# Performance work log

Hardware: AMD Instinct MI355X
Metric: run time of the kernel (lower is better)

Reference implementation:

```python
import jax, jax.numpy as jnp
import numpy as np

N = 50000      # nodes
E = 1600000    # edges (avg degree 32)
F_IN = 3       # PROTEINS num_node_features
H = 64         # dim_h
G = 512        # num graphs in batch
C = 2          # PROTEINS num_classes
BN_EPS = 1e-5


def setup_inputs() -> dict:
    key = jax.random.key(0)
    ks = iter(jax.random.split(key, 64))

    def rn(shape, s=0.1):
        return (jax.random.normal(next(ks), shape) * s).astype(jnp.float32)

    inp = {"x": rn((N, F_IN), 1.0)}
    for li, din in ((1, F_IN), (2, H), (3, H)):
        p = f"conv{li}_"
        inp[p + "w1"] = rn((din, H))
        inp[p + "b1"] = rn((H,))
        inp[p + "bn_g"] = jnp.ones((H,), jnp.float32)
        inp[p + "bn_b"] = jnp.zeros((H,), jnp.float32)
        inp[p + "bn_m"] = rn((H,))
        inp[p + "bn_v"] = jax.random.uniform(next(ks), (H,), jnp.float32, 0.5, 1.5)
        inp[p + "w2"] = rn((H, H))
        inp[p + "b2"] = rn((H,))
    inp["lin1_w"] = rn((3 * H, 3 * H))
    inp["lin1_b"] = rn((3 * H,))
    inp["lin2_w"] = rn((3 * H, C))
    inp["lin2_b"] = rn((C,))
    inp["edge_index"] = jax.random.randint(next(ks), (2, E), 0, N, jnp.int64)
    inp["batch"] = jnp.sort(jax.random.randint(next(ks), (N,), 0, G, jnp.int64))
    return inp


def gin_conv(x, src, dst, w1, b1, g, bb, m, v, w2, b2):
    # GINConv, eps=0: mlp(x + sum_{j->i} x_j); aggregate messages at target (dst)
    agg = jax.ops.segment_sum(x[src], dst, num_segments=N)  # [N, d]
    h = x + agg
    h = h @ w1 + b1
    h = (h - m) * jax.lax.rsqrt(v + BN_EPS) * g + bb  # BatchNorm1d (eval)
    h = jax.nn.relu(h)
    h = jax.nn.relu(h @ w2 + b2)
    return h


def reference(x,
              conv1_w1, conv1_b1, conv1_bn_g, conv1_bn_b, conv1_bn_m, conv1_bn_v, conv1_w2, conv1_b2,
              conv2_w1, conv2_b1, conv2_bn_g, conv2_bn_b, conv2_bn_m, conv2_bn_v, conv2_w2, conv2_b2,
              conv3_w1, conv3_b1, conv3_bn_g, conv3_bn_b, conv3_bn_m, conv3_bn_v, conv3_w2, conv3_b2,
              lin1_w, lin1_b, lin2_w, lin2_b,
              edge_index, batch):
    src, dst = edge_index[0], edge_index[1]
    h1 = gin_conv(x,  src, dst, conv1_w1, conv1_b1, conv1_bn_g, conv1_bn_b, conv1_bn_m, conv1_bn_v, conv1_w2, conv1_b2)
    h2 = gin_conv(h1, src, dst, conv2_w1, conv2_b1, conv2_bn_g, conv2_bn_b, conv2_bn_m, conv2_bn_v, conv2_w2, conv2_b2)
    h3 = gin_conv(h2, src, dst, conv3_w1, conv3_b1, conv3_bn_g, conv3_bn_b, conv3_bn_m, conv3_bn_v, conv3_w2, conv3_b2)
    # global_add_pool per graph
    p1 = jax.ops.segment_sum(h1, batch, num_segments=G)
    p2 = jax.ops.segment_sum(h2, batch, num_segments=G)
    p3 = jax.ops.segment_sum(h3, batch, num_segments=G)
    h = jnp.concatenate((p1, p2, p3), axis=1)          # [G, 3H]
    h = jax.nn.relu(h @ lin1_w + lin1_b)
    # dropout p=0.5 is identity in eval mode
    h = h @ lin2_w + lin2_b                            # [G, C]
    return (h, jax.nn.log_softmax(h, axis=1))
```

## Files before the change

### kernel.cpp

```cpp
#include <hip/hip_runtime.h>
#include <hip/hip_bf16.h>
#include <math.h>

#define N_NODES 50000
#define N_EDGES 1600000
#define H 64
#define G_GRAPHS 512
#define C_CLS 2
#define BN_EPS 1e-5f
#define NBUCK 196
#define E4 (N_EDGES / 4)
#define CSR_BLOCKS ((E4 + 511) / 512)

typedef __attribute__((ext_vector_type(8))) short short8;
typedef __attribute__((ext_vector_type(4))) float floatx4;

__device__ __forceinline__ float bflo(unsigned int u) { return __uint_as_float(u << 16); }
__device__ __forceinline__ float bfhi(unsigned int u) { return __uint_as_float(u & 0xffff0000u); }
__device__ __forceinline__ unsigned int bf16_rne(float f) {
    unsigned int u = __float_as_uint(f);
    u += 0x7fffu + ((u >> 16) & 1u);
    return u >> 16;
}

__global__ __launch_bounds__(256) void bhist_kernel(const int* __restrict__ dst,
                                                    int* __restrict__ gbh) {
    __shared__ int bh[NBUCK];
    int t = threadIdx.x;
    if (t < NBUCK) bh[t] = 0;
    __syncthreads();
    int base = blockIdx.x * 512;
#pragma unroll
    for (int p = 0; p < 2; p++) {
        int i = base + p * 256 + t;
        if (i < E4) {
            int4 d = ((const int4*)dst)[i];
            atomicAdd(&bh[d.x >> 8], 1);
            atomicAdd(&bh[d.y >> 8], 1);
            atomicAdd(&bh[d.z >> 8], 1);
            atomicAdd(&bh[d.w >> 8], 1);
        }
    }
    __syncthreads();
    if (t < NBUCK && bh[t]) atomicAdd(&gbh[t], bh[t]);
}

__global__ __launch_bounds__(256) void bscan_kernel(const int* __restrict__ gbh,
                                                    int* __restrict__ bucket_start,
                                                    int* __restrict__ cursor,
                                                    int* __restrict__ row_start) {
    __shared__ int s[256];
    int t = threadIdx.x;
    int v = (t < NBUCK) ? gbh[t] : 0;
    s[t] = v;
    __syncthreads();
    for (int off = 1; off < 256; off <<= 1) {
        int u = 0;
        if (t >= off) u = s[t - off];
        __syncthreads();
        if (t >= off) s[t] += u;
        __syncthreads();
    }
    int excl = s[t] - v;
    if (t < NBUCK) { bucket_start[t] = excl; cursor[t] = excl; }
    if (t == 0) { bucket_start[NBUCK] = N_EDGES; row_start[N_NODES] = N_EDGES; }
}

__global__ __launch_bounds__(256) void bscatter_kernel(const int* __restrict__ src,
                                                       const int* __restrict__ dst,
                                                       int* __restrict__ cursor,
                                                       int* __restrict__ gpacked) {
    __shared__ int bh[NBUCK];
    int t = threadIdx.x;
    if (t < NBUCK) bh[t] = 0;
    __syncthreads();
    int base = blockIdx.x * 512;

    int pkA[4], bkA[4], lrA[4]; bool vA = false;
    int pkB[4], bkB[4], lrB[4]; bool vB = false;
    {
        int i = base + t;
        if (i < E4) {
            vA = true;
            int4 s4 = ((const int4*)src)[i];
            int4 d4 = ((const int4*)dst)[i];
            bkA[0] = d4.x >> 8; pkA[0] = ((d4.x & 255) << 16) | s4.x; lrA[0] = atomicAdd(&bh[bkA[0]], 1);
            bkA[1] = d4.y >> 8; pkA[1] = ((d4.y & 255) << 16) | s4.y; lrA[1] = atomicAdd(&bh[bkA[1]], 1);
            bkA[2] = d4.z >> 8; pkA[2] = ((d4.z & 255) << 16) | s4.z; lrA[2] = atomicAdd(&bh[bkA[2]], 1);
            bkA[3] = d4.w >> 8; pkA[3] = ((d4.w & 255) << 16) | s4.w; lrA[3] = atomicAdd(&bh[bkA[3]], 1);
        }
    }
    {
        int i = base + 256 + t;
        if (i < E4) {
            vB = true;
            int4 s4 = ((const int4*)src)[i];
            int4 d4 = ((const int4*)dst)[i];
            bkB[0] = d4.x >> 8; pkB[0] = ((d4.x & 255) << 16) | s4.x; lrB[0] = atomicAdd(&bh[bkB[0]], 1);
            bkB[1] = d4.y >> 8; pkB[1] = ((d4.y & 255) << 16) | s4.y; lrB[1] = atomicAdd(&bh[bkB[1]], 1);
            bkB[2] = d4.z >> 8; pkB[2] = ((d4.z & 255) << 16) | s4.z; lrB[2] = atomicAdd(&bh[bkB[2]], 1);
            bkB[3] = d4.w >> 8; pkB[3] = ((d4.w & 255) << 16) | s4.w; lrB[3] = atomicAdd(&bh[bkB[3]], 1);
        }
    }
    __syncthreads();
    if (t < NBUCK) {
        int c = bh[t];
        bh[t] = c ? atomicAdd(&cursor[t], c) : 0;
    }
    __syncthreads();
    if (vA) {
#pragma unroll
        for (int q = 0; q < 4; q++) gpacked[bh[bkA[q]] + lrA[q]] = pkA[q];
    }
    if (vB) {
#pragma unroll
        for (int q = 0; q < 4; q++) gpacked[bh[bkB[q]] + lrB[q]] = pkB[q];
    }
}

__global__ __launch_bounds__(256) void bcsr_kernel(const int* __restrict__ gpacked,
                                                   const int* __restrict__ bucket_start,
                                                   int* __restrict__ row_start,
                                                   int* __restrict__ edge_src) {
    __shared__ int cnt[256];
    __shared__ int pref[256];
    int b = blockIdx.x;
    int t = threadIdx.x;
    int bs = bucket_start[b], be = bucket_start[b + 1];
    cnt[t] = 0;
    __syncthreads();
    for (int i = bs + t; i < be; i += 256) atomicAdd(&cnt[gpacked[i] >> 16], 1);
    __syncthreads();
    int v = cnt[t];
    pref[t] = v;
    __syncthreads();
    for (int off = 1; off < 256; off <<= 1) {
        int u = 0;
        if (t >= off) u = pref[t - off];
        __syncthreads();
        if (t >= off) pref[t] += u;
        __syncthreads();
    }
    int excl = pref[t] - v;
    int node = b * 256 + t;
    if (node < N_NODES) row_start[node] = bs + excl;
    cnt[t] = excl;
    __syncthreads();
    for (int i = bs + t; i < be; i += 256) {
        int p = gpacked[i];
        int pos = atomicAdd(&cnt[p >> 16], 1);
        edge_src[bs + pos] = p & 0xffff;
    }
}

__global__ __launch_bounds__(256) void gin_layer3_kernel(
    const float* __restrict__ x, const int* __restrict__ row_start,
    const int* __restrict__ edge_src,
    const float* __restrict__ w1, const float* __restrict__ b1,
    const float* __restrict__ bn_g, const float* __restrict__ bn_b,
    const float* __restrict__ bn_m, const float* __restrict__ bn_v,
    const float* __restrict__ w2, const float* __restrict__ b2,
    __hip_bfloat16* __restrict__ hout) {
    __shared__ float s_w1[3 * H];
    __shared__ float s_w2[H * H];
    __shared__ float s_mid[4][H];
    __shared__ float s_scale[H], s_shift[H], s_b1[H], s_b2[H];

    int tid = threadIdx.x;
    for (int i = tid; i < 3 * H; i += 256) s_w1[i] = w1[i];
    for (int i = tid; i < H * H; i += 256) s_w2[i] = w2[i];
    if (tid < H) {
        float sc = rsqrtf(bn_v[tid] + BN_EPS) * bn_g[tid];
        s_scale[tid] = sc;
        s_shift[tid] = bn_b[tid] - bn_m[tid] * sc;
        s_b1[tid] = b1[tid];
        s_b2[tid] = b2[tid];
    }
    __syncthreads();

    int wave = tid >> 6;
    int j = tid & 63;
    int node = blockIdx.x * 4 + wave;

    int rs = row_start[node], re = row_start[node + 1];
    float a0 = 0.f, a1 = 0.f, a2 = 0.f;
    for (int t = rs + j; t < re; t += 64) {
        int s = edge_src[t];
        a0 += x[s * 3 + 0];
        a1 += x[s * 3 + 1];
        a2 += x[s * 3 + 2];
    }
#pragma unroll
    for (int off = 32; off > 0; off >>= 1) {
        a0 += __shfl_xor(a0, off);
        a1 += __shfl_xor(a1, off);
        a2 += __shfl_xor(a2, off);
    }
    float in0 = a0 + x[node * 3 + 0];
    float in1 = a1 + x[node * 3 + 1];
    float in2 = a2 + x[node * 3 + 2];

    float m = s_b1[j] + in0 * s_w1[0 * H + j] + in1 * s_w1[1 * H + j] + in2 * s_w1[2 * H + j];
    m = m * s_scale[j] + s_shift[j];
    m = fmaxf(m, 0.f);
    s_mid[wave][j] = m;
    __syncthreads();
    float o = s_b2[j];
#pragma unroll
    for (int k = 0; k < H; k++) o += s_mid[wave][k] * s_w2[k * H + j];
    o = fmaxf(o, 0.f);
    hout[(size_t)node * H + j] = __float2bfloat16(o);
}

__global__ __launch_bounds__(512) void gather_kernel(
    const __hip_bfloat16* __restrict__ hin, const int* __restrict__ row_start,
    const int* __restrict__ edge_src, __hip_bfloat16* __restrict__ xs) {
    int tid = threadIdx.x;
    int wave = tid >> 6;
    int j = tid & 63;
    int o = j >> 3;
    int jo = j & 7;
    int node = blockIdx.x * 8 + wave;

    const char* hb = (const char*)hin;
    int rs = row_start[node], re = row_start[node + 1];
    float a0 = 0.f, a1 = 0.f, a2 = 0.f, a3 = 0.f, a4 = 0.f, a5 = 0.f, a6 = 0.f, a7 = 0.f;
    for (int base = rs; base < re; base += 64) {
        int idx = base + j;
        int sv = (idx < re) ? edge_src[idx] : 0;
        int cnt = min(64, re - base);
        int i = 0;
        for (; i + 8 <= cnt; i += 8) {
            int s = __shfl(sv, i + o);
            uint4 raw = *(const uint4*)(hb + (size_t)s * 128 + jo * 16);
            a0 += bflo(raw.x); a1 += bfhi(raw.x);
            a2 += bflo(raw.y); a3 += bfhi(raw.y);
            a4 += bflo(raw.z); a5 += bfhi(raw.z);
            a6 += bflo(raw.w); a7 += bfhi(raw.w);
        }
        if (i < cnt) {
            int r = cnt - i;
            int s = __shfl(sv, i + (o < r ? o : 0));
            uint4 raw = *(const uint4*)(hb + (size_t)s * 128 + jo * 16);
            if (o < r) {
                a0 += bflo(raw.x); a1 += bfhi(raw.x);
                a2 += bflo(raw.y); a3 += bfhi(raw.y);
                a4 += bflo(raw.z); a5 += bfhi(raw.z);
                a6 += bflo(raw.w); a7 += bfhi(raw.w);
            }
        }
    }
    a0 += __shfl_xor(a0, 8); a0 += __shfl_xor(a0, 16); a0 += __shfl_xor(a0, 32);
    a1 += __shfl_xor(a1, 8); a1 += __shfl_xor(a1, 16); a1 += __shfl_xor(a1, 32);
    a2 += __shfl_xor(a2, 8); a2 += __shfl_xor(a2, 16); a2 += __shfl_xor(a2, 32);
    a3 += __shfl_xor(a3, 8); a3 += __shfl_xor(a3, 16); a3 += __shfl_xor(a3, 32);
    a4 += __shfl_xor(a4, 8); a4 += __shfl_xor(a4, 16); a4 += __shfl_xor(a4, 32);
    a5 += __shfl_xor(a5, 8); a5 += __shfl_xor(a5, 16); a5 += __shfl_xor(a5, 32);
    a6 += __shfl_xor(a6, 8); a6 += __shfl_xor(a6, 16); a6 += __shfl_xor(a6, 32);
    a7 += __shfl_xor(a7, 8); a7 += __shfl_xor(a7, 16); a7 += __shfl_xor(a7, 32);
    if (o == 0) {
        uint4 raw = *(const uint4*)(hb + (size_t)node * 128 + jo * 16);
        a0 += bflo(raw.x); a1 += bfhi(raw.x);
        a2 += bflo(raw.y); a3 += bfhi(raw.y);
        a4 += bflo(raw.z); a5 += bfhi(raw.z);
        a6 += bflo(raw.w); a7 += bfhi(raw.w);
        uint4 ov;
        ov.x = bf16_rne(a0) | (bf16_rne(a1) << 16);
        ov.y = bf16_rne(a2) | (bf16_rne(a3) << 16);
        ov.z = bf16_rne(a4) | (bf16_rne(a5) << 16);
        ov.w = bf16_rne(a6) | (bf16_rne(a7) << 16);
        *(uint4*)((char*)xs + (size_t)node * 128 + jo * 16) = ov;
    }
}

#define IOP 72
__global__ __launch_bounds__(256) void mlp_mfma_kernel(
    const __hip_bfloat16* __restrict__ xs,
    const float* __restrict__ w1, const float* __restrict__ b1,
    const float* __restrict__ bn_g, const float* __restrict__ bn_b,
    const float* __restrict__ bn_m, const float* __restrict__ bn_v,
    const float* __restrict__ w2, const float* __restrict__ b2,
    __hip_bfloat16* __restrict__ hout) {
    __shared__ unsigned short s_w1t[H * IOP];
    __shared__ unsigned short s_w2t[H * IOP];
    __shared__ unsigned short s_mid[4][16 * IOP];
    __shared__ unsigned short s_out[4][16 * IOP];

    int tid = threadIdx.x;
    for (int idx = tid; idx < H * H; idx += 256) {
        int k = idx >> 6, jj = idx & 63;
        s_w1t[jj * IOP + k] = (unsigned short)bf16_rne(w1[idx]);
        s_w2t[jj * IOP + k] = (unsigned short)bf16_rne(w2[idx]);
    }
    int lane = tid & 63, wave = tid >> 6;
    int quad = lane >> 4, l15 = lane & 15;
    float scl[4], sht[4], bb1[4], bb2[4];
#pragma unroll
    for (int jt = 0; jt < 4; jt++) {
        int j = jt * 16 + l15;
        float sc = rsqrtf(bn_v[j] + BN_EPS) * bn_g[j];
        scl[jt] = sc;
        sht[jt] = bn_b[j] - bn_m[j] * sc;
        bb1[jt] = b1[j];
        bb2[jt] = b2[j];
    }
    __syncthreads();

    int base = blockIdx.x * 64 + wave * 16;
    const unsigned short* xr = (const unsigned short*)xs;
    int am = min(base + l15, N_NODES - 1);
    short8 a0 = *(const short8*)(xr + (size_t)am * H + quad * 8);
    short8 a1 = *(const short8*)(xr + (size_t)am * H + quad * 8 + 32);

    unsigned short* mid = s_mid[wave];
    unsigned short* outw = s_out[wave];

#pragma unroll
    for (int jt = 0; jt < 4; jt++) {
        short8 b0 = *(const short8*)&s_w1t[(jt * 16 + l15) * IOP + quad * 8];
        short8 bv = *(const short8*)&s_w1t[(jt * 16 + l15) * IOP + quad * 8 + 32];
        floatx4 c = {0.f, 0.f, 0.f, 0.f};
        c = __builtin_amdgcn_mfma_f32_16x16x32_bf16(a0, b0, c, 0, 0, 0);
        c = __builtin_amdgcn_mfma_f32_16x16x32_bf16(a1, bv, c, 0, 0, 0);
#pragma unroll
        for (int r = 0; r < 4; r++) {
            float v = (c[r] + bb1[jt]) * scl[jt] + sht[jt];
            v = fmaxf(v, 0.f);
            mid[(quad * 4 + r) * IOP + jt * 16 + l15] = (unsigned short)bf16_rne(v);
        }
    }
    __syncthreads();

    short8 m0 = *(const short8*)&mid[l15 * IOP + quad * 8];
    short8 m1 = *(const short8*)&mid[l15 * IOP + quad * 8 + 32];
#pragma unroll
    for (int jt = 0; jt < 4; jt++) {
        short8 b0 = *(const short8*)&s_w2t[(jt * 16 + l15) * IOP + quad * 8];
        short8 bv = *(const short8*)&s_w2t[(jt * 16 + l15) * IOP + quad * 8 + 32];
        floatx4 c = {0.f, 0.f, 0.f, 0.f};
        c = __builtin_amdgcn_mfma_f32_16x16x32_bf16(m0, b0, c, 0, 0, 0);
        c = __builtin_amdgcn_mfma_f32_16x16x32_bf16(m1, bv, c, 0, 0, 0);
#pragma unroll
        for (int r = 0; r < 4; r++) {
            float v = fmaxf(c[r] + bb2[jt], 0.f);
            outw[(quad * 4 + r) * IOP + jt * 16 + l15] = (unsigned short)bf16_rne(v);
        }
    }
    __syncthreads();

    unsigned short* ho = (unsigned short*)hout;
#pragma unroll
    for (int cc = 0; cc < 2; cc++) {
        int r = cc * 8 + (lane >> 3);
        int node = base + r;
        if (node < N_NODES) {
            short8 v = *(const short8*)&outw[r * IOP + (lane & 7) * 8];
            *(short8*)(ho + (size_t)node * H + (lane & 7) * 8) = v;
        }
    }
}

__global__ __launch_bounds__(192) void pool_head_kernel(
    const __hip_bfloat16* __restrict__ h1, const __hip_bfloat16* __restrict__ h2,
    const __hip_bfloat16* __restrict__ h3, const int* __restrict__ batch,
    const float* __restrict__ lin1_w, const float* __restrict__ lin1_b,
    const float* __restrict__ lin2_w, const float* __restrict__ lin2_b,
    float* __restrict__ out) {
    __shared__ float s_row[3 * H];
    __shared__ float s_mid[3 * H];
    __shared__ float s_z[C_CLS];
    __shared__ int s_se[2];

    int g = blockIdx.x;
    int j = threadIdx.x;
    if (j < 2) {
        int target = g + j;
        int lo = 0, hi = N_NODES;
        while (lo < hi) {
            int mid = (lo + hi) >> 1;
            if (batch[mid] < target) lo = mid + 1; else hi = mid;
        }
        s_se[j] = lo;
    }
    __syncthreads();
    int ns = s_se[0], ne = s_se[1];

    int which = j >> 6;
    int f = j & 63;
    const __hip_bfloat16* h = (which == 0) ? h1 : ((which == 1) ? h2 : h3);
    float p0 = 0.f, p1 = 0.f, p2 = 0.f, p3 = 0.f;
    int n = ns;
    for (; n + 3 < ne; n += 4) {
        p0 += __bfloat162float(h[(size_t)n * H + f]);
        p1 += __bfloat162float(h[(size_t)(n + 1) * H + f]);
        p2 += __bfloat162float(h[(size_t)(n + 2) * H + f]);
        p3 += __bfloat162float(h[(size_t)(n + 3) * H + f]);
    }
    for (; n < ne; n++) p0 += __bfloat162float(h[(size_t)n * H + f]);
    s_row[j] = (p0 + p1) + (p2 + p3);
    __syncthreads();

    float acc = lin1_b[j];
    for (int k = 0; k < 3 * H; k++) acc += s_row[k] * lin1_w[k * (3 * H) + j];
    s_mid[j] = fmaxf(acc, 0.f);
    __syncthreads();

    if (j < C_CLS) {
        float z = lin2_b[j];
        for (int k = 0; k < 3 * H; k++) z += s_mid[k] * lin2_w[k * C_CLS + j];
        s_z[j] = z;
    }
    __syncthreads();
    if (j < C_CLS) {
        float z0 = s_z[0], z1 = s_z[1];
        float mx = fmaxf(z0, z1);
        float lse = mx + logf(expf(z0 - mx) + expf(z1 - mx));
        out[g * C_CLS + j] = s_z[j];
        out[G_GRAPHS * C_CLS + g * C_CLS + j] = s_z[j] - lse;
    }
}

extern "C" void kernel_launch(void* const* d_in, const int* in_sizes, int n_in,
                              void* d_out, int out_size, void* d_ws, size_t ws_size,
                              hipStream_t stream) {
    const float* x = (const float*)d_in[0];
    const float* cw1[3], *cb1[3], *cg[3], *cbb[3], *cm[3], *cv[3], *cw2[3], *cb2[3];
    for (int l = 0; l < 3; l++) {
        int b = 1 + 8 * l;
        cw1[l] = (const float*)d_in[b + 0];
        cb1[l] = (const float*)d_in[b + 1];
        cg[l]  = (const float*)d_in[b + 2];
        cbb[l] = (const float*)d_in[b + 3];
        cm[l]  = (const float*)d_in[b + 4];
        cv[l]  = (const float*)d_in[b + 5];
        cw2[l] = (const float*)d_in[b + 6];
        cb2[l] = (const float*)d_in[b + 7];
    }
    const float* lin1_w = (const float*)d_in[25];
    const float* lin1_b = (const float*)d_in[26];
    const float* lin2_w = (const float*)d_in[27];
    const float* lin2_b = (const float*)d_in[28];
    const int* edge_index = (const int*)d_in[29];
    const int* batch = (const int*)d_in[30];
    const int* src = edge_index;
    const int* dst = edge_index + N_EDGES;
    float* out = (float*)d_out;

    int* edge_src = (int*)d_ws;
    int* gpacked = edge_src + N_EDGES;
    int* gbh = gpacked + N_EDGES;
    int* bucket_start = gbh + NBUCK;
    int* cursor = bucket_start + NBUCK + 1;
    int* row_start = cursor + NBUCK;
    uintptr_t hp = (uintptr_t)(row_start + N_NODES + 2);
    hp = (hp + 127) & ~(uintptr_t)127;
    __hip_bfloat16* h1 = (__hip_bfloat16*)hp;
    __hip_bfloat16* h2 = h1 + (size_t)N_NODES * H;
    __hip_bfloat16* h3 = h2 + (size_t)N_NODES * H;
    __hip_bfloat16* xs = h3 + (size_t)N_NODES * H;

    hipMemsetAsync(gbh, 0, NBUCK * sizeof(int), stream);
    bhist_kernel<<<CSR_BLOCKS, 256, 0, stream>>>(dst, gbh);
    bscan_kernel<<<1, 256, 0, stream>>>(gbh, bucket_start, cursor, row_start);
    bscatter_kernel<<<CSR_BLOCKS, 256, 0, stream>>>(src, dst, cursor, gpacked);
    bcsr_kernel<<<NBUCK, 256, 0, stream>>>(gpacked, bucket_start, row_start, edge_src);

    const int mlp_grid = (N_NODES + 63) / 64;

    gin_layer3_kernel<<<N_NODES / 4, 256, 0, stream>>>(x, row_start, edge_src,
        cw1[0], cb1[0], cg[0], cbb[0], cm[0], cv[0], cw2[0], cb2[0], h1);
    gather_kernel<<<N_NODES / 8, 512, 0, stream>>>(h1, row_start, edge_src, xs);
    mlp_mfma_kernel<<<mlp_grid, 256, 0, stream>>>(xs,
        cw1[1], cb1[1], cg[1], cbb[1], cm[1], cv[1], cw2[1], cb2[1], h2);
    gather_kernel<<<N_NODES / 8, 512, 0, stream>>>(h2, row_start, edge_src, xs);
    mlp_mfma_kernel<<<mlp_grid, 256, 0, stream>>>(xs,
        cw1[2], cb1[2], cg[2], cbb[2], cm[2], cv[2], cw2[2], cb2[2], h3);
    pool_head_kernel<<<G_GRAPHS, 3 * H, 0, stream>>>(h1, h2, h3, batch,
        lin1_w, lin1_b, lin2_w, lin2_b, out);
}
```

Measured before the change: 329.9 us.

## Split layer-1 GIN into gather+first-linear kernel and MFMA second-linear kernel

```diff
diff --git a/kernel.cpp b/kernel.cpp
--- a/kernel.cpp
+++ b/kernel.cpp
@@ -153,34 +153,17 @@
     }
 }
 
-__global__ __launch_bounds__(256) void gin_layer3_kernel(
+__global__ __launch_bounds__(512) void gather3_mid_kernel(
     const float* __restrict__ x, const int* __restrict__ row_start,
     const int* __restrict__ edge_src,
     const float* __restrict__ w1, const float* __restrict__ b1,
     const float* __restrict__ bn_g, const float* __restrict__ bn_b,
     const float* __restrict__ bn_m, const float* __restrict__ bn_v,
-    const float* __restrict__ w2, const float* __restrict__ b2,
-    __hip_bfloat16* __restrict__ hout) {
-    __shared__ float s_w1[3 * H];
-    __shared__ float s_w2[H * H];
-    __shared__ float s_mid[4][H];
-    __shared__ float s_scale[H], s_shift[H], s_b1[H], s_b2[H];
-
+    __hip_bfloat16* __restrict__ mid) {
     int tid = threadIdx.x;
-    for (int i = tid; i < 3 * H; i += 256) s_w1[i] = w1[i];
-    for (int i = tid; i < H * H; i += 256) s_w2[i] = w2[i];
-    if (tid < H) {
-        float sc = rsqrtf(bn_v[tid] + BN_EPS) * bn_g[tid];
-        s_scale[tid] = sc;
-        s_shift[tid] = bn_b[tid] - bn_m[tid] * sc;
-        s_b1[tid] = b1[tid];
-        s_b2[tid] = b2[tid];
-    }
-    __syncthreads();
-
     int wave = tid >> 6;
     int j = tid & 63;
-    int node = blockIdx.x * 4 + wave;
+    int node = blockIdx.x * 8 + wave;
 
     int rs = row_start[node], re = row_start[node + 1];
     float a0 = 0.f, a1 = 0.f, a2 = 0.f;
@@ -200,16 +183,65 @@
     float in1 = a1 + x[node * 3 + 1];
     float in2 = a2 + x[node * 3 + 2];
 
-    float m = s_b1[j] + in0 * s_w1[0 * H + j] + in1 * s_w1[1 * H + j] + in2 * s_w1[2 * H + j];
-    m = m * s_scale[j] + s_shift[j];
-    m = fmaxf(m, 0.f);
-    s_mid[wave][j] = m;
-    __syncthreads();
-    float o = s_b2[j];
-#pragma unroll
-    for (int k = 0; k < H; k++) o += s_mid[wave][k] * s_w2[k * H + j];
-    o = fmaxf(o, 0.f);
-    hout[(size_t)node * H + j] = __float2bfloat16(o);
+    float sc = rsqrtf(bn_v[j] + BN_EPS) * bn_g[j];
+    float sh = bn_b[j] - bn_m[j] * sc;
+    float m = b1[j] + in0 * w1[j] + in1 * w1[H + j] + in2 * w1[2 * H + j];
+    m = fmaxf(m * sc + sh, 0.f);
+    ((unsigned short*)mid)[(size_t)node * H + j] = (unsigned short)bf16_rne(m);
+}
+
+#define IOP 72
+__global__ __launch_bounds__(256) void matmul2_mfma_kernel(
+    const __hip_bfloat16* __restrict__ xin,
+    const float* __restrict__ w2, const float* __restrict__ b2,
+    __hip_bfloat16* __restrict__ hout) {
+    __shared__ unsigned short s_w2t[H * IOP];
+    __shared__ unsigned short s_out[4][16 * IOP];
+
+    int tid = threadIdx.x;
+    for (int idx = tid; idx < H * H; idx += 256) {
+        int k = idx >> 6, jj = idx & 63;
+        s_w2t[jj * IOP + k] = (unsigned short)bf16_rne(w2[idx]);
+    }
+    int lane = tid & 63, wave = tid >> 6;
+    int quad = lane >> 4, l15 = lane & 15;
+    float bb2[4];
+#pragma unroll
+    for (int jt = 0; jt < 4; jt++) bb2[jt] = b2[jt * 16 + l15];
+    __syncthreads();
+
+    int base = blockIdx.x * 64 + wave * 16;
+    const unsigned short* xr = (const unsigned short*)xin;
+    int am = min(base + l15, N_NODES - 1);
+    short8 a0 = *(const short8*)(xr + (size_t)am * H + quad * 8);
+    short8 a1 = *(const short8*)(xr + (size_t)am * H + quad * 8 + 32);
+
+    unsigned short* outw = s_out[wave];
+#pragma unroll
+    for (int jt = 0; jt < 4; jt++) {
+        short8 b0 = *(const short8*)&s_w2t[(jt * 16 + l15) * IOP + quad * 8];
+        short8 bv = *(const short8*)&s_w2t[(jt * 16 + l15) * IOP + quad * 8 + 32];
+        floatx4 c = {0.f, 0.f, 0.f, 0.f};
+        c = __builtin_amdgcn_mfma_f32_16x16x32_bf16(a0, b0, c, 0, 0, 0);
+        c = __builtin_amdgcn_mfma_f32_16x16x32_bf16(a1, bv, c, 0, 0, 0);
+#pragma unroll
+        for (int r = 0; r < 4; r++) {
+            float v = fmaxf(c[r] + bb2[jt], 0.f);
+            outw[(quad * 4 + r) * IOP + jt * 16 + l15] = (unsigned short)bf16_rne(v);
+        }
+    }
+    __syncthreads();
+
+    unsigned short* ho = (unsigned short*)hout;
+#pragma unroll
+    for (int cc = 0; cc < 2; cc++) {
+        int r = cc * 8 + (lane >> 3);
+        int node = base + r;
+        if (node < N_NODES) {
+            short8 v = *(const short8*)&outw[r * IOP + (lane & 7) * 8];
+            *(short8*)(ho + (size_t)node * H + (lane & 7) * 8) = v;
+        }
+    }
 }
 
 __global__ __launch_bounds__(512) void gather_kernel(
@@ -273,7 +305,6 @@
     }
 }
 
-#define IOP 72
 __global__ __launch_bounds__(256) void mlp_mfma_kernel(
     const __hip_bfloat16* __restrict__ xs,
     const float* __restrict__ w1, const float* __restrict__ b1,
@@ -467,8 +498,9 @@
 
     const int mlp_grid = (N_NODES + 63) / 64;
 
-    gin_layer3_kernel<<<N_NODES / 4, 256, 0, stream>>>(x, row_start, edge_src,
-        cw1[0], cb1[0], cg[0], cbb[0], cm[0], cv[0], cw2[0], cb2[0], h1);
+    gather3_mid_kernel<<<N_NODES / 8, 512, 0, stream>>>(x, row_start, edge_src,
+        cw1[0], cb1[0], cg[0], cbb[0], cm[0], cv[0], xs);
+    matmul2_mfma_kernel<<<mlp_grid, 256, 0, stream>>>(xs, cw2[0], cb2[0], h1);
     gather_kernel<<<N_NODES / 8, 512, 0, stream>>>(h1, row_start, edge_src, xs);
     mlp_mfma_kernel<<<mlp_grid, 256, 0, stream>>>(xs,
         cw1[1], cb1[1], cg[1], cbb[1], cm[1], cv[1], cw2[1], cb2[1], h2);
```

Result: faster. 310.2 us (-6.0%).
